# Optimization experiments

Measured on AMD Instinct MI355X. Metric: run time of the kernel, lower is better.

## Reference

```python
import jax, jax.numpy as jnp
import numpy as np
import math

DIM_EMB = 1024
DIM_QK = 1024
DIM_V = 1024
NORM_FACT = 1.0 / math.sqrt(DIM_EMB)

def setup_inputs() -> dict:
    key = jax.random.key(0)
    k0, k1, k2, k3 = jax.random.split(key, 4)
    x = jax.random.normal(k0, (4, 4096, DIM_EMB), dtype=jnp.float32)
    # nn.Linear weights are [out_features, in_features]; y = x @ W.T
    s = 1.0 / math.sqrt(DIM_EMB)
    Wq = jax.random.uniform(k1, (DIM_QK, DIM_EMB), jnp.float32, -s, s)
    Wk = jax.random.uniform(k2, (DIM_QK, DIM_EMB), jnp.float32, -s, s)
    Wv = jax.random.uniform(k3, (DIM_V, DIM_EMB), jnp.float32, -s, s)
    return {"x": x, "Wq": Wq, "Wk": Wk, "Wv": Wv}

def reference(x, Wq, Wk, Wv):
    # q,k,v: [b, n, d]
    q = jnp.einsum('bne,de->bnd', x, Wq)
    k = jnp.einsum('bne,de->bnd', x, Wk)
    v = jnp.einsum('bne,de->bnd', x, Wv)
    logits = jnp.einsum('bnd,bmd->bnm', q, k)  # [b, n, n]
    # Faithful to source: softmax over last dim FIRST, then scale by 1/sqrt(dim_embedding)
    score = jax.nn.softmax(logits, axis=-1) * NORM_FACT
    att = jnp.einsum('bnm,bmv->bnv', score, v)
    return att
```

## Files before the change

### kernel.cpp

```cpp
#include <hip/hip_runtime.h>
#include <hip/hip_bf16.h>

typedef _Float16 f16;
typedef _Float16 f16x4 __attribute__((ext_vector_type(4)));
typedef _Float16 f16x8 __attribute__((ext_vector_type(8)));
typedef float f32x4 __attribute__((ext_vector_type(4)));

__device__ __forceinline__ void gload16(const void* g, void* l) {
    __builtin_amdgcn_global_load_lds(
        (const __attribute__((address_space(1))) void*)g,
        (__attribute__((address_space(3))) void*)l, 16, 0, 0);
}

template<bool F16IN, bool F16OUT, bool PIPE>
__global__ __launch_bounds__(256) void gemm_bt(
    const void* __restrict__ Av, const void* __restrict__ Bv, void* __restrict__ Cv,
    int K, int lda, int ldb, int ldc, float scale)
{
    constexpr int NB = PIPE ? 2 : 1;
    __shared__ f16 sA[NB][128 * 64];
    __shared__ f16 sB[NB][128 * 64];
    const int tid = threadIdx.x, lane = tid & 63, wid = tid >> 6;
    const int wr = wid >> 1, wc = wid & 1;
    const int bm = blockIdx.x * 128, bn = blockIdx.y * 128;

    f32x4 acc[4][4] = {};

    auto stage16 = [&](int kt, int bsel) {
        const f16* A = (const f16*)Av;
        const f16* B = (const f16*)Bv;
        const int rsub = lane >> 3;
        const int csw = ((lane & 7) ^ rsub) << 3;
#pragma unroll
        for (int i = 0; i < 4; ++i) {
            const int rb = (wid * 4 + i) * 8;
            gload16(A + (size_t)(bm + rb + rsub) * lda + kt + csw, &sA[bsel][rb * 64]);
            gload16(B + (size_t)(bn + rb + rsub) * ldb + kt + csw, &sB[bsel][rb * 64]);
        }
    };

    auto compute = [&](int bsel) {
#pragma unroll
        for (int ks = 0; ks < 2; ++ks) {
            const int kk = ks * 32 + (lane >> 4) * 8;
            f16x8 a[4], b[4];
#pragma unroll
            for (int i = 0; i < 4; ++i) {
                const int ra = wr * 64 + i * 16 + (lane & 15);
                a[i] = *(const f16x8*)(&sA[bsel][(ra << 6) + (kk ^ ((ra & 7) << 3))]);
                const int rb2 = wc * 64 + i * 16 + (lane & 15);
                b[i] = *(const f16x8*)(&sB[bsel][(rb2 << 6) + (kk ^ ((rb2 & 7) << 3))]);
            }
#pragma unroll
            for (int i = 0; i < 4; ++i)
#pragma unroll
                for (int j = 0; j < 4; ++j)
                    acc[i][j] = __builtin_amdgcn_mfma_f32_16x16x32_f16(a[i], b[j], acc[i][j], 0, 0, 0);
        }
    };

    if constexpr (PIPE) {
        static_assert(F16IN, "PIPE requires f16 inputs");
        stage16(0, 0);
        asm volatile("s_waitcnt vmcnt(0)" ::: "memory");
        __syncthreads();
        const int NT2 = K >> 6;
        for (int t = 0; t < NT2; ++t) {
            if (t + 1 < NT2) stage16((t + 1) << 6, (t + 1) & 1);
            compute(t & 1);
            asm volatile("s_waitcnt vmcnt(0)" ::: "memory");
            __builtin_amdgcn_s_barrier();
        }
    } else {
        for (int kt = 0; kt < K; kt += 64) {
            __syncthreads();
            if constexpr (F16IN) {
                stage16(kt, 0);
            } else {
                const float* A = (const float*)Av;
                const float* B = (const float*)Bv;
                const int r0 = tid >> 4;
                const int c4 = (tid & 15) << 2;
#pragma unroll
                for (int p = 0; p < 8; ++p) {
                    const int row = (p << 4) + r0;
                    const float4 av = *(const float4*)(A + (size_t)(bm + row) * lda + kt + c4);
                    const float4 bv = *(const float4*)(B + (size_t)(bn + row) * ldb + kt + c4);
                    const int sc = c4 ^ ((row & 7) << 3);
                    f16x4 ah = { (f16)av.x, (f16)av.y, (f16)av.z, (f16)av.w };
                    f16x4 bh = { (f16)bv.x, (f16)bv.y, (f16)bv.z, (f16)bv.w };
                    *(f16x4*)(&sA[0][(row << 6) + sc]) = ah;
                    *(f16x4*)(&sB[0][(row << 6) + sc]) = bh;
                }
            }
            __syncthreads();
            compute(0);
        }
    }
#pragma unroll
    for (int i = 0; i < 4; ++i)
#pragma unroll
        for (int j = 0; j < 4; ++j)
#pragma unroll
            for (int r = 0; r < 4; ++r) {
                const int row = bm + wr * 64 + i * 16 + (lane >> 4) * 4 + r;
                const int col = bn + wc * 64 + j * 16 + (lane & 15);
                if constexpr (F16OUT)
                    ((f16*)Cv)[(size_t)row * ldc + col] = (f16)acc[i][j][r];
                else
                    ((float*)Cv)[(size_t)row * ldc + col] = acc[i][j][r] * scale;
            }
}

__global__ __launch_bounds__(256) void cvt_f16(
    const float* __restrict__ s, f16* __restrict__ d, int n8)
{
    int i = blockIdx.x * 256 + threadIdx.x;
    const int stride = gridDim.x * 256;
    for (; i < n8; i += stride) {
        const float4 a = ((const float4*)s)[i * 2];
        const float4 b = ((const float4*)s)[i * 2 + 1];
        f16x8 o = { (f16)a.x, (f16)a.y, (f16)a.z, (f16)a.w,
                    (f16)b.x, (f16)b.y, (f16)b.z, (f16)b.w };
        ((f16x8*)d)[i] = o;
    }
}

__global__ __launch_bounds__(256) void softmax_inplace(float* S)
{
    const int lane = threadIdx.x & 63, wid = threadIdx.x >> 6;
    const int row = blockIdx.x * 4 + wid;
    float* src = S + (size_t)row * 4096;
    float4 v[16];
#pragma unroll
    for (int u = 0; u < 16; ++u)
        v[u] = ((const float4*)src)[u * 64 + lane];
    float m = -1e30f;
#pragma unroll
    for (int u = 0; u < 16; ++u)
        m = fmaxf(m, fmaxf(fmaxf(v[u].x, v[u].y), fmaxf(v[u].z, v[u].w)));
#pragma unroll
    for (int msk = 1; msk <= 32; msk <<= 1) m = fmaxf(m, __shfl_xor(m, msk));
    float s = 0.f;
#pragma unroll
    for (int u = 0; u < 16; ++u) {
        v[u].x = __expf(v[u].x - m); v[u].y = __expf(v[u].y - m);
        v[u].z = __expf(v[u].z - m); v[u].w = __expf(v[u].w - m);
        s += (v[u].x + v[u].y) + (v[u].z + v[u].w);
    }
#pragma unroll
    for (int msk = 1; msk <= 32; msk <<= 1) s += __shfl_xor(s, msk);
    const float inv = 1.0f / s;
    f16* dst = (f16*)S + (size_t)row * 8192;
#pragma unroll
    for (int u = 0; u < 16; ++u) {
        f16x4 p = { (f16)(v[u].x * inv), (f16)(v[u].y * inv),
                    (f16)(v[u].z * inv), (f16)(v[u].w * inv) };
        *(f16x4*)(dst + u * 256 + lane * 4) = p;
    }
}

extern "C" void kernel_launch(void* const* d_in, const int* in_sizes, int n_in,
                              void* d_out, int out_size, void* d_ws, size_t ws_size,
                              hipStream_t stream) {
    const float* x  = (const float*)d_in[0];
    const float* Wq = (const float*)d_in[1];
    const float* Wk = (const float*)d_in[2];
    const float* Wv = (const float*)d_in[3];
    float* out = (float*)d_out;

    f16*   qk  = (f16*)d_out;
    f16*   xh  = (f16*)d_ws;
    f16*   wqh = xh + 16384LL * 1024;
    f16*   wkh = wqh + 1024LL * 1024;
    float* Sf  = (float*)d_ws;
    f16*   Sh  = (f16*)d_ws;

    cvt_f16<<<1024, 256, 0, stream>>>(x,  xh,  16384 * 1024 / 8);
    cvt_f16<<<512,  256, 0, stream>>>(Wq, wqh, 1024 * 1024 / 8);
    cvt_f16<<<512,  256, 0, stream>>>(Wk, wkh, 1024 * 1024 / 8);

    gemm_bt<true, true, false><<<dim3(128, 8), 256, 0, stream>>>(
        xh, wqh, qk,        1024, 1024, 1024, 2048, 1.f);
    gemm_bt<true, true, false><<<dim3(128, 8), 256, 0, stream>>>(
        xh, wkh, qk + 1024, 1024, 1024, 1024, 2048, 1.f);

    for (int b = 0; b < 4; ++b) {
        const size_t tb = (size_t)b * 4096;
        gemm_bt<true, false, false><<<dim3(32, 32), 256, 0, stream>>>(
            qk + tb * 2048, qk + tb * 2048 + 1024, Sf,
            1024, 2048, 2048, 4096, 1.f);
        softmax_inplace<<<1024, 256, 0, stream>>>(Sf);
        gemm_bt<false, true, false><<<dim3(8, 32), 256, 0, stream>>>(
            Wv, x + tb * 1024, Sh + 3072LL * 8192 + 4096,
            1024, 1024, 1024, 8192, 1.f);
        gemm_bt<true, false, true><<<dim3(32, 8), 256, 0, stream>>>(
            Sh, Sh + 3072LL * 8192 + 4096, out + tb * 1024,
            4096, 8192, 8192, 1024, 1.f / 32.f);
    }
}
```

Baseline: 683.1 us.

## Add 256x256-tile 8-wave pipelined GEMM for projections and QK^T

```diff
diff --git a/kernel.cpp b/kernel.cpp
--- a/kernel.cpp
+++ b/kernel.cpp
@@ -10,6 +10,114 @@
     __builtin_amdgcn_global_load_lds(
         (const __attribute__((address_space(1))) void*)g,
         (__attribute__((address_space(3))) void*)l, 16, 0, 0);
+}
+
+#define FENCE asm volatile("" ::: "memory")
+#define BARRIER do { FENCE; __builtin_amdgcn_s_barrier(); FENCE; } while (0)
+
+#define PHASE_MFMA(QI, QJ)                                                    \
+    __builtin_amdgcn_s_setprio(1);                                            \
+    _Pragma("unroll")                                                         \
+    for (int ks = 0; ks < 2; ++ks)                                            \
+      _Pragma("unroll")                                                       \
+      for (int i = 0; i < 4; ++i)                                             \
+        _Pragma("unroll")                                                     \
+        for (int j = 0; j < 2; ++j)                                           \
+          acc[(QI)*4 + i][(QJ)*2 + j] = __builtin_amdgcn_mfma_f32_16x16x32_f16( \
+              a[i][ks], b[j][ks], acc[(QI)*4 + i][(QJ)*2 + j], 0, 0, 0);      \
+    __builtin_amdgcn_s_setprio(0);
+
+template<bool F16OUT>
+__global__ __launch_bounds__(512) void gemm_bt8(
+    const f16* __restrict__ A, const f16* __restrict__ B, void* __restrict__ Cv,
+    int K, int lda, int ldb, int ldc, float scale, int nbn)
+{
+    __shared__ f16 sA[2][256 * 64];
+    __shared__ f16 sB[2][256 * 64];
+    const int tid = threadIdx.x, lane = tid & 63, wid = tid >> 6;
+    const int wr = wid >> 2, wc = wid & 3;
+
+    const int cpx = gridDim.x >> 3;
+    const int wg = (blockIdx.x & 7) * cpx + (blockIdx.x >> 3);
+    const int bm = (wg / nbn) << 8, bn = (wg % nbn) << 8;
+
+    const int rr8 = lane >> 3;
+    const int cs  = ((lane & 7) ^ rr8) << 3;
+    const int ldsr = wid << 3;
+
+    auto stageA = [&](int kt, int c, int h) {
+        const size_t g0 = (size_t)(bm + (h << 7) + ldsr + rr8) * lda + kt + cs;
+        gload16(A + g0,                      &sA[c][((h << 7) + ldsr) << 6]);
+        gload16(A + g0 + ((size_t)lda << 6), &sA[c][((h << 7) + 64 + ldsr) << 6]);
+    };
+    auto stageB = [&](int kt, int c, int h) {
+        const size_t g0 = (size_t)(bn + (h << 7) + ldsr + rr8) * ldb + kt + cs;
+        gload16(B + g0,                      &sB[c][((h << 7) + ldsr) << 6]);
+        gload16(B + g0 + ((size_t)ldb << 6), &sB[c][((h << 7) + 64 + ldsr) << 6]);
+    };
+
+    f32x4 acc[8][4] = {};
+    f16x8 a[4][2], b[2][2];
+
+    auto loadA = [&](int c, int qi) {
+#pragma unroll
+        for (int i = 0; i < 4; ++i) {
+            const int ra = wr * 128 + (qi * 4 + i) * 16 + (lane & 15);
+            const int swz = (ra & 7) << 3;
+#pragma unroll
+            for (int ks = 0; ks < 2; ++ks) {
+                const int kk = ks * 32 + (lane >> 4) * 8;
+                a[i][ks] = *(const f16x8*)(&sA[c][(ra << 6) + (kk ^ swz)]);
+            }
+        }
+    };
+    auto loadB = [&](int c, int qj) {
+#pragma unroll
+        for (int j = 0; j < 2; ++j) {
+            const int rb = wc * 64 + (qj * 2 + j) * 16 + (lane & 15);
+            const int swz = (rb & 7) << 3;
+#pragma unroll
+            for (int ks = 0; ks < 2; ++ks) {
+                const int kk = ks * 32 + (lane >> 4) * 8;
+                b[j][ks] = *(const f16x8*)(&sB[c][(rb << 6) + (kk ^ swz)]);
+            }
+        }
+    };
+
+    stageA(0, 0, 0); stageA(0, 0, 1); stageB(0, 0, 0); stageB(0, 0, 1);
+    asm volatile("s_waitcnt vmcnt(0)" ::: "memory");
+    BARRIER;
+
+    const int NT = K >> 6;
+    for (int g = 0; g < NT; ++g) {
+        const int c = g & 1, cn = c ^ 1;
+        const int kn = (g + 1) << 6;
+        const bool more = (g + 1) < NT;
+        loadA(c, 0); loadB(c, 0);
+        if (more) { stageA(kn, cn, 0); stageA(kn, cn, 1); }
+        BARRIER; PHASE_MFMA(0, 0); BARRIER;
+        loadB(c, 1);
+        if (more) { stageB(kn, cn, 0); stageB(kn, cn, 1); }
+        BARRIER; PHASE_MFMA(0, 1); BARRIER;
+        loadA(c, 1); loadB(c, 0);
+        BARRIER; PHASE_MFMA(1, 0); BARRIER;
+        loadB(c, 1);
+        asm volatile("s_waitcnt vmcnt(0)" ::: "memory");
+        BARRIER; PHASE_MFMA(1, 1); BARRIER;
+    }
+#pragma unroll
+    for (int i = 0; i < 8; ++i)
+#pragma unroll
+        for (int j = 0; j < 4; ++j)
+#pragma unroll
+            for (int r = 0; r < 4; ++r) {
+                const int row = bm + wr * 128 + i * 16 + ((lane >> 4) << 2) + r;
+                const int col = bn + wc * 64 + j * 16 + (lane & 15);
+                if constexpr (F16OUT)
+                    ((f16*)Cv)[(size_t)row * ldc + col] = (f16)(acc[i][j][r] * scale);
+                else
+                    ((float*)Cv)[(size_t)row * ldc + col] = acc[i][j][r] * scale;
+            }
 }
 
 template<bool F16IN, bool F16OUT, bool PIPE>
@@ -180,16 +288,14 @@
     cvt_f16<<<512,  256, 0, stream>>>(Wq, wqh, 1024 * 1024 / 8);
     cvt_f16<<<512,  256, 0, stream>>>(Wk, wkh, 1024 * 1024 / 8);
 
-    gemm_bt<true, true, false><<<dim3(128, 8), 256, 0, stream>>>(
-        xh, wqh, qk,        1024, 1024, 1024, 2048, 1.f);
-    gemm_bt<true, true, false><<<dim3(128, 8), 256, 0, stream>>>(
-        xh, wkh, qk + 1024, 1024, 1024, 1024, 2048, 1.f);
+    gemm_bt8<true><<<256, 512, 0, stream>>>(xh, wqh, qk,        1024, 1024, 1024, 2048, 1.f, 4);
+    gemm_bt8<true><<<256, 512, 0, stream>>>(xh, wkh, qk + 1024, 1024, 1024, 1024, 2048, 1.f, 4);
 
     for (int b = 0; b < 4; ++b) {
         const size_t tb = (size_t)b * 4096;
-        gemm_bt<true, false, false><<<dim3(32, 32), 256, 0, stream>>>(
+        gemm_bt8<false><<<256, 512, 0, stream>>>(
             qk + tb * 2048, qk + tb * 2048 + 1024, Sf,
-            1024, 2048, 2048, 4096, 1.f);
+            1024, 2048, 2048, 4096, 1.f, 16);
         softmax_inplace<<<1024, 256, 0, stream>>>(Sf);
         gemm_bt<false, true, false><<<dim3(8, 32), 256, 0, stream>>>(
             Wv, x + tb * 1024, Sh + 3072LL * 8192 + 4096,
```

After: 649.9 us. 4.9% less time.

## Add 256x256 eight-wave GEMM with split-K atomics for PV and f16 V projection

Applied to the files above, without the earlier changes.

```diff
diff --git a/kernel.cpp b/kernel.cpp
--- a/kernel.cpp
+++ b/kernel.cpp
@@ -10,6 +10,138 @@
     __builtin_amdgcn_global_load_lds(
         (const __attribute__((address_space(1))) void*)g,
         (__attribute__((address_space(3))) void*)l, 16, 0, 0);
+}
+
+#define FENCE asm volatile("" ::: "memory")
+#define BARRIER do { FENCE; __builtin_amdgcn_s_barrier(); FENCE; } while (0)
+
+#define PHASE_MFMA(QI, QJ)                                                    \
+    __builtin_amdgcn_s_setprio(1);                                            \
+    _Pragma("unroll")                                                         \
+    for (int ks = 0; ks < 2; ++ks)                                            \
+      _Pragma("unroll")                                                       \
+      for (int i = 0; i < 4; ++i)                                             \
+        _Pragma("unroll")                                                     \
+        for (int j = 0; j < 2; ++j)                                           \
+          acc[(QI)*4 + i][(QJ)*2 + j] = __builtin_amdgcn_mfma_f32_16x16x32_f16( \
+              a[i][ks], b[j][ks], acc[(QI)*4 + i][(QJ)*2 + j], 0, 0, 0);      \
+    __builtin_amdgcn_s_setprio(0);
+
+#define BT8_BODY(KBASE, NTILES)                                               \
+    const int rr8 = lane >> 3;                                                \
+    const int cs  = ((lane & 7) ^ rr8) << 3;                                  \
+    const int ldsr = wid << 3;                                                \
+    auto stageA = [&](int kt, int c, int h) {                                 \
+        const size_t g0 = (size_t)(bm + (h << 7) + ldsr + rr8) * lda + (KBASE) + kt + cs; \
+        gload16(A + g0,                      &sA[c][((h << 7) + ldsr) << 6]); \
+        gload16(A + g0 + ((size_t)lda << 6), &sA[c][((h << 7) + 64 + ldsr) << 6]); \
+    };                                                                        \
+    auto stageB = [&](int kt, int c, int h) {                                 \
+        const size_t g0 = (size_t)(bn + (h << 7) + ldsr + rr8) * ldb + (KBASE) + kt + cs; \
+        gload16(B + g0,                      &sB[c][((h << 7) + ldsr) << 6]); \
+        gload16(B + g0 + ((size_t)ldb << 6), &sB[c][((h << 7) + 64 + ldsr) << 6]); \
+    };                                                                        \
+    f32x4 acc[8][4] = {};                                                     \
+    f16x8 a[4][2], b[2][2];                                                   \
+    auto loadA = [&](int c, int qi) {                                         \
+        _Pragma("unroll")                                                     \
+        for (int i = 0; i < 4; ++i) {                                         \
+            const int ra = wr * 128 + (qi * 4 + i) * 16 + (lane & 15);        \
+            const int swz = (ra & 7) << 3;                                    \
+            _Pragma("unroll")                                                 \
+            for (int ks = 0; ks < 2; ++ks) {                                  \
+                const int kk = ks * 32 + (lane >> 4) * 8;                     \
+                a[i][ks] = *(const f16x8*)(&sA[c][(ra << 6) + (kk ^ swz)]);   \
+            }                                                                 \
+        }                                                                     \
+    };                                                                        \
+    auto loadB = [&](int c, int qj) {                                         \
+        _Pragma("unroll")                                                     \
+        for (int j = 0; j < 2; ++j) {                                         \
+            const int rb = wc * 64 + (qj * 2 + j) * 16 + (lane & 15);         \
+            const int swz = (rb & 7) << 3;                                    \
+            _Pragma("unroll")                                                 \
+            for (int ks = 0; ks < 2; ++ks) {                                  \
+                const int kk = ks * 32 + (lane >> 4) * 8;                     \
+                b[j][ks] = *(const f16x8*)(&sB[c][(rb << 6) + (kk ^ swz)]);   \
+            }                                                                 \
+        }                                                                     \
+    };                                                                        \
+    stageA(0, 0, 0); stageA(0, 0, 1); stageB(0, 0, 0); stageB(0, 0, 1);       \
+    asm volatile("s_waitcnt vmcnt(0)" ::: "memory");                          \
+    BARRIER;                                                                  \
+    for (int g = 0; g < (NTILES); ++g) {                                      \
+        const int c = g & 1, cn = c ^ 1;                                      \
+        const int kn = (g + 1) << 6;                                          \
+        const bool more = (g + 1) < (NTILES);                                 \
+        loadA(c, 0); loadB(c, 0);                                             \
+        if (more) { stageA(kn, cn, 0); stageA(kn, cn, 1); }                   \
+        BARRIER; PHASE_MFMA(0, 0); BARRIER;                                   \
+        loadB(c, 1);                                                          \
+        if (more) { stageB(kn, cn, 0); stageB(kn, cn, 1); }                   \
+        BARRIER; PHASE_MFMA(0, 1); BARRIER;                                   \
+        loadA(c, 1); loadB(c, 0);                                             \
+        BARRIER; PHASE_MFMA(1, 0); BARRIER;                                   \
+        loadB(c, 1);                                                          \
+        asm volatile("s_waitcnt vmcnt(0)" ::: "memory");                      \
+        BARRIER; PHASE_MFMA(1, 1); BARRIER;                                   \
+    }
+
+template<bool F16OUT>
+__global__ __launch_bounds__(512) void gemm_bt8(
+    const f16* __restrict__ A, const f16* __restrict__ B, void* __restrict__ Cv,
+    int K, int lda, int ldb, int ldc, float scale, int nbn)
+{
+    __shared__ f16 sA[2][256 * 64];
+    __shared__ f16 sB[2][256 * 64];
+    const int tid = threadIdx.x, lane = tid & 63, wid = tid >> 6;
+    const int wr = wid >> 2, wc = wid & 3;
+    const int cpx = gridDim.x >> 3;
+    const int wg = (blockIdx.x & 7) * cpx + (blockIdx.x >> 3);
+    const int bm = (wg / nbn) << 8, bn = (wg % nbn) << 8;
+
+    BT8_BODY(0, K >> 6)
+
+#pragma unroll
+    for (int i = 0; i < 8; ++i)
+#pragma unroll
+        for (int j = 0; j < 4; ++j)
+#pragma unroll
+            for (int r = 0; r < 4; ++r) {
+                const int row = bm + wr * 128 + i * 16 + ((lane >> 4) << 2) + r;
+                const int col = bn + wc * 64 + j * 16 + (lane & 15);
+                if constexpr (F16OUT)
+                    ((f16*)Cv)[(size_t)row * ldc + col] = (f16)(acc[i][j][r] * scale);
+                else
+                    ((float*)Cv)[(size_t)row * ldc + col] = acc[i][j][r] * scale;
+            }
+}
+
+__global__ __launch_bounds__(512) void gemm_pv8(
+    const f16* __restrict__ A, const f16* __restrict__ B, float* __restrict__ C,
+    int lda, int ldb, int ldc, float scale)
+{
+    __shared__ f16 sA[2][256 * 64];
+    __shared__ f16 sB[2][256 * 64];
+    const int tid = threadIdx.x, lane = tid & 63, wid = tid >> 6;
+    const int wr = wid >> 2, wc = wid & 3;
+    const int cpx = gridDim.x >> 3;
+    const int wg = (blockIdx.x & 7) * cpx + (blockIdx.x >> 3);
+    const int bm = (wg >> 2) << 8, bn = (wg & 3) << 8;
+    const int kbase = blockIdx.y << 10;
+
+    BT8_BODY(kbase, 16)
+
+#pragma unroll
+    for (int i = 0; i < 8; ++i)
+#pragma unroll
+        for (int j = 0; j < 4; ++j)
+#pragma unroll
+            for (int r = 0; r < 4; ++r) {
+                const int row = bm + wr * 128 + i * 16 + ((lane >> 4) << 2) + r;
+                const int col = bn + wc * 64 + j * 16 + (lane & 15);
+                atomicAdd(&C[(size_t)row * ldc + col], acc[i][j][r] * scale);
+            }
 }
 
 template<bool F16IN, bool F16OUT, bool PIPE>
@@ -60,7 +192,6 @@
     };
 
     if constexpr (PIPE) {
-        static_assert(F16IN, "PIPE requires f16 inputs");
         stage16(0, 0);
         asm volatile("s_waitcnt vmcnt(0)" ::: "memory");
         __syncthreads();
@@ -74,25 +205,7 @@
     } else {
         for (int kt = 0; kt < K; kt += 64) {
             __syncthreads();
-            if constexpr (F16IN) {
-                stage16(kt, 0);
-            } else {
-                const float* A = (const float*)Av;
-                const float* B = (const float*)Bv;
-                const int r0 = tid >> 4;
-                const int c4 = (tid & 15) << 2;
-#pragma unroll
-                for (int p = 0; p < 8; ++p) {
-                    const int row = (p << 4) + r0;
-                    const float4 av = *(const float4*)(A + (size_t)(bm + row) * lda + kt + c4);
-                    const float4 bv = *(const float4*)(B + (size_t)(bn + row) * ldb + kt + c4);
-                    const int sc = c4 ^ ((row & 7) << 3);
-                    f16x4 ah = { (f16)av.x, (f16)av.y, (f16)av.z, (f16)av.w };
-                    f16x4 bh = { (f16)bv.x, (f16)bv.y, (f16)bv.z, (f16)bv.w };
-                    *(f16x4*)(&sA[0][(row << 6) + sc]) = ah;
-                    *(f16x4*)(&sB[0][(row << 6) + sc]) = bh;
-                }
-            }
+            stage16(kt, 0);
             __syncthreads();
             compute(0);
         }
@@ -126,6 +239,14 @@
     }
 }
 
+__global__ __launch_bounds__(256) void zerof(float* __restrict__ p, int n4)
+{
+    int i = blockIdx.x * 256 + threadIdx.x;
+    const int stride = gridDim.x * 256;
+    const float4 z = {0.f, 0.f, 0.f, 0.f};
+    for (; i < n4; i += stride) ((float4*)p)[i] = z;
+}
+
 __global__ __launch_bounds__(256) void softmax_inplace(float* S)
 {
     const int lane = threadIdx.x & 63, wid = threadIdx.x >> 6;
@@ -175,27 +296,29 @@
     f16*   wkh = wqh + 1024LL * 1024;
     float* Sf  = (float*)d_ws;
     f16*   Sh  = (f16*)d_ws;
+    f16*   vTp = Sh + 3072LL * 8192 + 4096;
 
     cvt_f16<<<1024, 256, 0, stream>>>(x,  xh,  16384 * 1024 / 8);
     cvt_f16<<<512,  256, 0, stream>>>(Wq, wqh, 1024 * 1024 / 8);
     cvt_f16<<<512,  256, 0, stream>>>(Wk, wkh, 1024 * 1024 / 8);
 
-    gemm_bt<true, true, false><<<dim3(128, 8), 256, 0, stream>>>(
-        xh, wqh, qk,        1024, 1024, 1024, 2048, 1.f);
-    gemm_bt<true, true, false><<<dim3(128, 8), 256, 0, stream>>>(
-        xh, wkh, qk + 1024, 1024, 1024, 1024, 2048, 1.f);
+    gemm_bt8<true><<<256, 512, 0, stream>>>(xh, wqh, qk,        1024, 1024, 1024, 2048, 1.f, 4);
+    gemm_bt8<true><<<256, 512, 0, stream>>>(xh, wkh, qk + 1024, 1024, 1024, 1024, 2048, 1.f, 4);
 
     for (int b = 0; b < 4; ++b) {
         const size_t tb = (size_t)b * 4096;
-        gemm_bt<true, false, false><<<dim3(32, 32), 256, 0, stream>>>(
+        f16* xhb = (f16*)(out + tb * 1024);
+        f16* wvh = xhb + 4096LL * 1024;
+        gemm_bt8<false><<<256, 512, 0, stream>>>(
             qk + tb * 2048, qk + tb * 2048 + 1024, Sf,
-            1024, 2048, 2048, 4096, 1.f);
+            1024, 2048, 2048, 4096, 1.f, 16);
         softmax_inplace<<<1024, 256, 0, stream>>>(Sf);
-        gemm_bt<false, true, false><<<dim3(8, 32), 256, 0, stream>>>(
-            Wv, x + tb * 1024, Sh + 3072LL * 8192 + 4096,
-            1024, 1024, 1024, 8192, 1.f);
-        gemm_bt<true, false, true><<<dim3(32, 8), 256, 0, stream>>>(
-            Sh, Sh + 3072LL * 8192 + 4096, out + tb * 1024,
-            4096, 8192, 8192, 1024, 1.f / 32.f);
-    }
-}
+        cvt_f16<<<1024, 256, 0, stream>>>(x + tb * 1024, xhb, 4096 * 1024 / 8);
+        cvt_f16<<<512,  256, 0, stream>>>(Wv, wvh, 1024 * 1024 / 8);
+        gemm_bt<true, true, true><<<dim3(8, 32), 256, 0, stream>>>(
+            wvh, xhb, vTp, 1024, 1024, 1024, 8192, 1.f);
+        zerof<<<2048, 256, 0, stream>>>(out + tb * 1024, 4096 * 1024 / 4);
+        gemm_pv8<<<dim3(64, 4), 512, 0, stream>>>(
+            Sh, vTp, out + tb * 1024, 8192, 8192, 1024, 1.f / 32.f);
+    }
+}
```

Result: slower. 768.4 us (+12.5%).
